# Optimization experiments

Hardware: AMD Instinct MI355X
Metric: run time of the kernel (lower is better)

The kernel has to match this reference:

```python
import jax, jax.numpy as jnp
import numpy as np

ROUTER_TEMP = 1.0
SCALING = 16.0 / 8.0  # lora_alpha / r


def setup_inputs() -> dict:
    key = jax.random.key(0)
    ks = jax.random.split(key, 6)
    B, S, D, O, E, R = 4, 2048, 4096, 4096, 8, 8
    return {
        "x": jax.random.normal(ks[0], (B, S, D), dtype=jnp.float32),
        "W_base": jax.random.normal(ks[1], (O, D), dtype=jnp.float32) * 0.02,
        "b_base": jax.random.normal(ks[2], (O,), dtype=jnp.float32) * 0.02,
        "lora_A": jax.random.normal(ks[3], (E, R, D), dtype=jnp.float32) * 0.02,
        "lora_B": jax.random.normal(ks[4], (E, O, R), dtype=jnp.float32) * 0.02,
        "router_W": jax.random.normal(ks[5], (E, D), dtype=jnp.float32) * 0.02,
        "router_b": jnp.zeros((E,), dtype=jnp.float32),
    }


def reference(x, W_base, b_base, lora_A, lora_B, router_W, router_b):
    # Base linear: [B,S,D] @ [D,O] + b -> [B,S,O]
    result = jnp.einsum("bsd,od->bso", x, W_base) + b_base

    # Router over mean-pooled sequence: [B,D] -> [B,E]
    x_router = x.mean(axis=1)
    logits = jnp.einsum("bd,ed->be", x_router, router_W) + router_b
    weights = jax.nn.softmax(logits / ROUTER_TEMP, axis=-1)  # [B,E]

    # Per-expert LoRA: down-project to small r, weight by router, up-project.
    h = jnp.einsum("bsd,erd->bser", x, lora_A)            # [B,S,E,r] (small)
    hw = h * weights[:, None, :, None]                      # router-weighted
    lora_out = jnp.einsum("bser,eor->bso", hw, lora_B)     # [B,S,O]

    return result + lora_out * SCALING
```

## Files before the change

kernel.cpp:

```cpp
#include <hip/hip_runtime.h>
#include <hip/hip_bf16.h>


typedef unsigned short u16;
typedef __attribute__((ext_vector_type(8))) short short8;
typedef __attribute__((ext_vector_type(8))) unsigned short u16x8;
typedef __attribute__((ext_vector_type(4))) float f32x4;

#define AS1(p) ((const __attribute__((address_space(1))) void*)(p))
#define AS3(p) ((__attribute__((address_space(3))) void*)(p))

constexpr int KM   = 4224;
constexpr int NOUT = 4096;

__device__ __forceinline__ u16 f2bf(float f) {
    union { float f; unsigned int u; } v; v.f = f;
    unsigned int r = v.u + 0x7fffu + ((v.u >> 16) & 1u);
    return (u16)(r >> 16);
}

__global__ __launch_bounds__(256) void k_convx(const float* __restrict__ x,
                                               u16* __restrict__ Xext,
                                               float* __restrict__ colpart) {
    const int t = threadIdx.x;
    const int row0 = (blockIdx.x >> 7) * 2048 + (blockIdx.x & 127) * 16;
    float4 cs[4] = {{0,0,0,0},{0,0,0,0},{0,0,0,0},{0,0,0,0}};
    for (int r = 0; r < 16; ++r) {
        size_t roff = (size_t)(row0 + r) * 4096;
        #pragma unroll
        for (int g = 0; g < 2; ++g) {
            int col = g * 2048 + t * 8;
            const float4* p = (const float4*)(x + roff + col);
            float4 v0 = p[0], v1 = p[1];
            cs[2*g].x += v0.x; cs[2*g].y += v0.y; cs[2*g].z += v0.z; cs[2*g].w += v0.w;
            cs[2*g+1].x += v1.x; cs[2*g+1].y += v1.y; cs[2*g+1].z += v1.z; cs[2*g+1].w += v1.w;
            u16x8 o;
            o[0]=f2bf(v0.x); o[1]=f2bf(v0.y); o[2]=f2bf(v0.z); o[3]=f2bf(v0.w);
            o[4]=f2bf(v1.x); o[5]=f2bf(v1.y); o[6]=f2bf(v1.z); o[7]=f2bf(v1.w);
            *(u16x8*)(Xext + (size_t)(row0 + r) * KM + col) = o;
        }
    }
    float* cp = colpart + (size_t)blockIdx.x * 4096;
    #pragma unroll
    for (int g = 0; g < 2; ++g) {
        *(float4*)(cp + g * 2048 + t * 8)     = cs[2*g];
        *(float4*)(cp + g * 2048 + t * 8 + 4) = cs[2*g+1];
    }
}

__global__ __launch_bounds__(256) void k_red(const float* __restrict__ colpart,
                                             float* __restrict__ colsum) {
    const int b = blockIdx.x >> 4;
    const int col = (blockIdx.x & 15) * 256 + threadIdx.x;
    const float* p = colpart + (size_t)b * 128 * 4096 + col;
    float acc = 0.f;
    #pragma unroll 4
    for (int sc = 0; sc < 128; ++sc) acc += p[(size_t)sc * 4096];
    colsum[b * 4096 + col] = acc;
}

__global__ __launch_bounds__(256) void k_lgt(const float* __restrict__ colsum,
                                             const float* __restrict__ rW,
                                             float* __restrict__ logits) {
    const int b = blockIdx.x >> 3, e = blockIdx.x & 7;
    const int t = threadIdx.x;
    const float4* cp = (const float4*)(colsum + b * 4096 + t * 16);
    const float4* wp = (const float4*)(rW + e * 4096 + t * 16);
    float acc = 0.f;
    #pragma unroll
    for (int j = 0; j < 4; ++j) {
        float4 c = cp[j], w = wp[j];
        acc += c.x * w.x + c.y * w.y + c.z * w.z + c.w * w.w;
    }
    __shared__ float red[256];
    red[t] = acc;
    __syncthreads();
    for (int off = 128; off > 0; off >>= 1) {
        if (t < off) red[t] += red[t + off];
        __syncthreads();
    }
    if (t == 0) logits[b * 8 + e] = red[0];
}

__global__ void k_conv8(const float* __restrict__ src, u16* __restrict__ dst) {
    size_t t = (size_t)blockIdx.x * 256 + threadIdx.x;
    size_t base = t * 8;
    size_t row = base >> 12;
    int col = (int)(base & 4095);
    const float4* s = (const float4*)(src + base);
    float4 v0 = s[0], v1 = s[1];
    u16x8 o;
    o[0]=f2bf(v0.x); o[1]=f2bf(v0.y); o[2]=f2bf(v0.z); o[3]=f2bf(v0.w);
    o[4]=f2bf(v1.x); o[5]=f2bf(v1.y); o[6]=f2bf(v1.z); o[7]=f2bf(v1.w);
    *(u16x8*)(dst + row * KM + col) = o;
}

__global__ void k_wlora(const float* __restrict__ lb, u16* __restrict__ Wext) {
    int f = blockIdx.x * 256 + threadIdx.x;
    int e = f >> 15, o = (f >> 3) & 4095, r = f & 7;
    Wext[(size_t)o * KM + 4096 + e * 8 + r] = f2bf(lb[f]);
    Wext[(size_t)(f >> 6) * KM + 4160 + (f & 63)] = 0;
}

__global__ void k_abf(const float* __restrict__ la, u16* __restrict__ Abf) {
    int f = blockIdx.x * 256 + threadIdx.x;
    Abf[f] = f2bf(la[f]);
}

__global__ __launch_bounds__(256) void k_hgemm(const u16* __restrict__ Xb,
                                               const u16* __restrict__ Ab,
                                               const float* __restrict__ logits,
                                               const float* __restrict__ rb,
                                               u16* __restrict__ Hout) {
    __shared__ u16 As[8 * 1024];
    __shared__ u16 Bs[8 * 2048];
    __shared__ float Red[4 * 2048];
    __shared__ float wscL[8];
    const int tid = threadIdx.x, lane = tid & 63, w = tid >> 6;
    const int m0 = blockIdx.x * 32;
    const int b = blockIdx.x >> 6;

    if (tid < 8) {
        float l[8], mx = -1e30f;
        #pragma unroll
        for (int j = 0; j < 8; ++j) {
            l[j] = logits[b * 8 + j] * (1.0f / 2048.0f) + rb[j];
            mx = fmaxf(mx, l[j]);
        }
        float s = 0.f;
        #pragma unroll
        for (int j = 0; j < 8; ++j) s += expf(l[j] - mx);
        wscL[tid] = 2.0f * expf(l[tid] - mx) / s;
    }
    asm volatile("s_waitcnt vmcnt(0)" ::: "memory");

    f32x4 acc[2][4] = {};
    const int kbase = w * 1024;

    auto issue = [&](int it, int buf) {
        const int kt = kbase + it * 32;
        u16* Aw = As + (w * 2 + buf) * 1024;
        u16* Bw = Bs + (w * 2 + buf) * 2048;
        #pragma unroll
        for (int i = 0; i < 2; ++i) {
            int f = lane + i * 64;
            __builtin_amdgcn_global_load_lds(
                AS1(Xb + (size_t)(m0 + (f >> 2)) * KM + kt + (f & 3) * 8),
                AS3(Aw + f * 8), 16, 0, 0);
        }
        #pragma unroll
        for (int i = 0; i < 4; ++i) {
            int f = lane + i * 64;
            __builtin_amdgcn_global_load_lds(
                AS1(Ab + (size_t)(f >> 2) * 4096 + kt + (f & 3) * 8),
                AS3(Bw + f * 8), 16, 0, 0);
        }
    };

    issue(0, 0);
    for (int it = 0; it < 32; ++it) {
        const int buf = it & 1;
        if (it + 1 < 32) {
            issue(it + 1, buf ^ 1);
            asm volatile("s_waitcnt vmcnt(6)" ::: "memory");
        } else {
            asm volatile("s_waitcnt vmcnt(0)" ::: "memory");
        }
        const u16* Aw = As + (w * 2 + buf) * 1024;
        const u16* Bw = Bs + (w * 2 + buf) * 2048;
        short8 af[2], bfr[4];
        #pragma unroll
        for (int mi = 0; mi < 2; ++mi)
            af[mi] = *(const short8*)(Aw + (mi * 16 + (lane & 15)) * 32 + (lane >> 4) * 8);
        #pragma unroll
        for (int nj = 0; nj < 4; ++nj)
            bfr[nj] = *(const short8*)(Bw + (nj * 16 + (lane & 15)) * 32 + (lane >> 4) * 8);
        #pragma unroll
        for (int mi = 0; mi < 2; ++mi)
            #pragma unroll
            for (int nj = 0; nj < 4; ++nj)
                acc[mi][nj] = __builtin_amdgcn_mfma_f32_16x16x32_bf16(af[mi], bfr[nj], acc[mi][nj], 0, 0, 0);
        asm volatile("" ::: "memory");
    }

    const int quad = lane >> 4, lcol = lane & 15;
    #pragma unroll
    for (int mi = 0; mi < 2; ++mi)
        #pragma unroll
        for (int nj = 0; nj < 4; ++nj)
            #pragma unroll
            for (int r = 0; r < 4; ++r)
                Red[w * 2048 + (mi * 16 + quad * 4 + r) * 64 + nj * 16 + lcol] = acc[mi][nj][r];
    __syncthreads();

    const int o = tid * 8, row = o >> 6, col = o & 63;
    float s0=0,s1=0,s2=0,s3=0,s4=0,s5=0,s6=0,s7=0;
    #pragma unroll
    for (int ww = 0; ww < 4; ++ww) {
        const float4* p = (const float4*)(Red + ww * 2048 + o);
        float4 v0 = p[0], v1 = p[1];
        s0+=v0.x; s1+=v0.y; s2+=v0.z; s3+=v0.w;
        s4+=v1.x; s5+=v1.y; s6+=v1.z; s7+=v1.w;
    }
    const float wgt = wscL[col >> 3];
    u16x8 out;
    out[0]=f2bf(s0*wgt); out[1]=f2bf(s1*wgt); out[2]=f2bf(s2*wgt); out[3]=f2bf(s3*wgt);
    out[4]=f2bf(s4*wgt); out[5]=f2bf(s5*wgt); out[6]=f2bf(s6*wgt); out[7]=f2bf(s7*wgt);
    *(u16x8*)(Hout + (size_t)(m0 + row) * KM + 4096 + col) = out;
    u16x8 zz = {0,0,0,0,0,0,0,0};
    *(u16x8*)(Hout + (size_t)(m0 + (tid >> 3)) * KM + 4160 + (tid & 7) * 8) = zz;
}


#define LDB_(bufB) do { \
    const char* bp_ = ldsc + bBaseB + (bufB); \
    _Pragma("unroll") \
    for (int nj_ = 0; nj_ < 4; ++nj_) { \
        bf[nj_][0] = *(const short8*)(bp_ + nj_ * 2048 + rdk0); \
        bf[nj_][1] = *(const short8*)(bp_ + nj_ * 2048 + rdk1); \
    } \
} while (0)

#define LDA_(bufB, pq) do { \
    const char* ap_ = ldsc + aBaseB + (bufB) + (pq) * 4096; \
    af[0][0] = *(const short8*)(ap_ + rdk0); \
    af[0][1] = *(const short8*)(ap_ + rdk1); \
    af[1][0] = *(const short8*)(ap_ + 2048 + rdk0); \
    af[1][1] = *(const short8*)(ap_ + 2048 + rdk1); \
} while (0)

#define MFMA_(pq) do { \
    __builtin_amdgcn_s_barrier(); \
    asm volatile("s_waitcnt lgkmcnt(0)" ::: "memory"); \
    __builtin_amdgcn_sched_barrier(0); \
    __builtin_amdgcn_s_setprio(1); \
    _Pragma("unroll") \
    for (int k_ = 0; k_ < 2; ++k_) \
        _Pragma("unroll") \
        for (int q_ = 0; q_ < 2; ++q_) \
            _Pragma("unroll") \
            for (int nj_ = 0; nj_ < 4; ++nj_) \
                acc[(pq)*2+q_][nj_] = __builtin_amdgcn_mfma_f32_16x16x32_bf16(af[q_][k_], bf[nj_][k_], acc[(pq)*2+q_][nj_], 0, 0, 0); \
    __builtin_amdgcn_s_setprio(0); \
    __builtin_amdgcn_sched_barrier(0); \
} while (0)

#define ENDPH_() __builtin_amdgcn_s_barrier()
#define VM_(n)   asm volatile("s_waitcnt vmcnt(" #n ")" ::: "memory")

__global__ __launch_bounds__(512, 2) void k_main(const u16* __restrict__ A, const u16* __restrict__ B,
                                                 const float* __restrict__ bias, float* __restrict__ C) {
    __shared__ __align__(16) u16 lds[65536];
    const char* ldsc = (const char*)lds;
    const int tid = threadIdx.x;
    const int lane = tid & 63;
    const int w = tid >> 6;
    const int wm = w >> 2;
    const int wn = w & 3;
    const int lr = lane & 15, hi = lane >> 4;

    const int bid = blockIdx.x;
    const int swz = (bid & 7) * 64 + (bid >> 3);
    const int m0 = (swz >> 4) * 256;
    const int n0 = (swz & 15) * 256;

    const int csw = (lr & 7) << 4;
    const int rdk0 = lr * 128 + ((hi * 16) ^ csw);
    const int rdk1 = lr * 128 + ((64 + hi * 16) ^ csw);
    const int aBaseB = wm * 16384;
    const int bBaseB = 32768 + (wn >> 1) * 16384 + (wn & 1) * 8192;

    const int srow = tid >> 3;
    const int scol = ((tid & 7) ^ ((tid >> 3) & 7)) * 8;
    const int so0 = srow * KM + scol;
    const int so1 = (64 + srow) * KM + scol;
    const u16* Am0 = A + (size_t)m0 * KM;
    const u16* Am1 = A + (size_t)(m0 + 128) * KM;
    const u16* Bm0 = B + (size_t)n0 * KM;
    const u16* Bm1 = B + (size_t)(n0 + 128) * KM;
    u16* ldst = lds + tid * 8;

    auto stageB = [&](const u16* src, int t, int regionEl) {
        __builtin_amdgcn_global_load_lds(AS1(src + so0 + t * 64), AS3(ldst + regionEl), 16, 0, 0);
        __builtin_amdgcn_global_load_lds(AS1(src + so1 + t * 64), AS3(ldst + regionEl + 4096), 16, 0, 0);
    };
    auto stageA = [&](int t, int bufEl, int which) {
        const size_t ro = (size_t)(which * 64) * KM;
        __builtin_amdgcn_global_load_lds(AS1(Am0 + ro + so0 + t * 64),
                                         AS3(ldst + bufEl + which * 4096), 16, 0, 0);
        __builtin_amdgcn_global_load_lds(AS1(Am1 + ro + so0 + t * 64),
                                         AS3(ldst + bufEl + 8192 + which * 4096), 16, 0, 0);
    };

    f32x4 acc[8][4] = {};

    stageB(Bm0, 0, 16384);
    stageB(Bm1, 0, 24576);
    stageA(0, 0, 0);
    stageA(0, 0, 1);
    stageB(Bm0, 1, 32768 + 16384);
    stageB(Bm1, 1, 32768 + 24576);
    VM_(6);
    __builtin_amdgcn_s_barrier();

    #pragma unroll 1
    for (int i = 0; i < 33; ++i) {
        const int t = i * 2;
        const bool nl = (i < 32);
        short8 af[2][2];
        short8 bf[4][2];
        LDB_(0); LDA_(0, 0);
        stageA(t + 1, 32768, 0);
        MFMA_(0); ENDPH_();
        LDA_(0, 1);
        stageA(t + 1, 32768, 1);
        MFMA_(1); VM_(8); ENDPH_();
        LDA_(0, 2);
        if (nl) stageB(Bm0, t + 2, 16384);
        MFMA_(2); ENDPH_();
        LDA_(0, 3);
        if (nl) stageB(Bm1, t + 2, 24576);
        MFMA_(3);
        if (nl) { VM_(6); } else { VM_(2); }
        ENDPH_();
        LDB_(65536); LDA_(65536, 0);
        if (nl) stageA(t + 2, 0, 0);
        MFMA_(0); ENDPH_();
        LDA_(65536, 1);
        if (nl) stageA(t + 2, 0, 1);
        MFMA_(1);
        if (nl) { VM_(8); } else { VM_(0); }
        ENDPH_();
        LDA_(65536, 2);
        if (nl) stageB(Bm0, t + 3, 32768 + 16384);
        MFMA_(2); ENDPH_();
        LDA_(65536, 3);
        if (nl) stageB(Bm1, t + 3, 32768 + 24576);
        MFMA_(3);
        if (nl) { VM_(6); }
        ENDPH_();
    }

    const int colb = n0 + wn * 64 + lr;
    const int rowb = m0 + wm * 128 + hi * 4;
    #pragma unroll
    for (int nj = 0; nj < 4; ++nj) {
        const int col = colb + nj * 16;
        const float bv = bias[col];
        #pragma unroll
        for (int mi = 0; mi < 8; ++mi) {
            float* Cp = C + (size_t)(rowb + mi * 16) * NOUT + col;
            #pragma unroll
            for (int r = 0; r < 4; ++r)
                Cp[(size_t)r * NOUT] = acc[mi][nj][r] + bv;
        }
    }
}

extern "C" void kernel_launch(void* const* d_in, const int* in_sizes, int n_in,
                              void* d_out, int out_size, void* d_ws, size_t ws_size,
                              hipStream_t stream) {
    const float* x  = (const float*)d_in[0];
    const float* Wb = (const float*)d_in[1];
    const float* bb = (const float*)d_in[2];
    const float* lA = (const float*)d_in[3];
    const float* lB = (const float*)d_in[4];
    const float* rW = (const float*)d_in[5];
    const float* rb = (const float*)d_in[6];
    float* out = (float*)d_out;

    char* ws = (char*)d_ws;
    float* logits = (float*)ws;
    u16* Abf      = (u16*)(ws + 256);
    u16* Xext     = (u16*)(ws + 524800);
    u16* Wext     = (u16*)(ws + 524800 + 69206016ULL);
    float* colpart = (float*)Wext;
    float* colsum  = (float*)((char*)Wext + (16u << 20));

    k_abf   <<<1024, 256, 0, stream>>>(lA, Abf);
    k_convx <<<512,  256, 0, stream>>>(x, Xext, colpart);
    k_red   <<<64,   256, 0, stream>>>(colpart, colsum);
    k_lgt   <<<32,   256, 0, stream>>>(colsum, rW, logits);
    k_hgemm <<<256,  256, 0, stream>>>(Xext, Abf, logits, rb, Xext);
    k_conv8 <<<8192, 256, 0, stream>>>(Wb, Wext);
    k_wlora <<<1024, 256, 0, stream>>>(lB, Wext);
    k_main  <<<512,  512, 0, stream>>>(Xext, Wext, bb, out);
}
```

Baseline: 552.0 us.

## Switch main GEMM to 32x32x16 MFMA tiles and double convx grid

The main bf16 GEMM's inner loop now issues 32x32x16 MFMA instructions instead of 16x16x32. LDS fragment reads, accumulator layout and the epilogue store mapping are reworked to match. The aim is fewer MFMA issues and fewer LDS fragment loads per tile, which raises arithmetic intensity per wave. Separately, the x-conversion kernel now uses 1024 blocks of 8 rows instead of 512 blocks of 16, for more parallelism, at the cost of a longer column-partial reduction and a larger colpart buffer.

```diff
diff --git a/kernel.cpp b/kernel.cpp
--- a/kernel.cpp
+++ b/kernel.cpp
@@ -6,6 +6,7 @@
 typedef __attribute__((ext_vector_type(8))) short short8;
 typedef __attribute__((ext_vector_type(8))) unsigned short u16x8;
 typedef __attribute__((ext_vector_type(4))) float f32x4;
+typedef __attribute__((ext_vector_type(16))) float f32x16;
 
 #define AS1(p) ((const __attribute__((address_space(1))) void*)(p))
 #define AS3(p) ((__attribute__((address_space(3))) void*)(p))
@@ -23,9 +24,9 @@
                                                u16* __restrict__ Xext,
                                                float* __restrict__ colpart) {
     const int t = threadIdx.x;
-    const int row0 = (blockIdx.x >> 7) * 2048 + (blockIdx.x & 127) * 16;
+    const int row0 = (blockIdx.x >> 8) * 2048 + (blockIdx.x & 255) * 8;
     float4 cs[4] = {{0,0,0,0},{0,0,0,0},{0,0,0,0},{0,0,0,0}};
-    for (int r = 0; r < 16; ++r) {
+    for (int r = 0; r < 8; ++r) {
         size_t roff = (size_t)(row0 + r) * 4096;
         #pragma unroll
         for (int g = 0; g < 2; ++g) {
@@ -52,10 +53,10 @@
                                              float* __restrict__ colsum) {
     const int b = blockIdx.x >> 4;
     const int col = (blockIdx.x & 15) * 256 + threadIdx.x;
-    const float* p = colpart + (size_t)b * 128 * 4096 + col;
+    const float* p = colpart + (size_t)b * 256 * 4096 + col;
     float acc = 0.f;
-    #pragma unroll 4
-    for (int sc = 0; sc < 128; ++sc) acc += p[(size_t)sc * 4096];
+    #pragma unroll 8
+    for (int sc = 0; sc < 256; ++sc) acc += p[(size_t)sc * 4096];
     colsum[b * 4096 + col] = acc;
 }
 
@@ -215,18 +216,17 @@
 #define LDB_(bufB) do { \
     const char* bp_ = ldsc + bBaseB + (bufB); \
     _Pragma("unroll") \
-    for (int nj_ = 0; nj_ < 4; ++nj_) { \
-        bf[nj_][0] = *(const short8*)(bp_ + nj_ * 2048 + rdk0); \
-        bf[nj_][1] = *(const short8*)(bp_ + nj_ * 2048 + rdk1); \
-    } \
+    for (int nj_ = 0; nj_ < 2; ++nj_) \
+        _Pragma("unroll") \
+        for (int ks_ = 0; ks_ < 4; ++ks_) \
+            bf[nj_][ks_] = *(const short8*)(bp_ + nj_ * 4096 + ardk[ks_]); \
 } while (0)
 
 #define LDA_(bufB, pq) do { \
     const char* ap_ = ldsc + aBaseB + (bufB) + (pq) * 4096; \
-    af[0][0] = *(const short8*)(ap_ + rdk0); \
-    af[0][1] = *(const short8*)(ap_ + rdk1); \
-    af[1][0] = *(const short8*)(ap_ + 2048 + rdk0); \
-    af[1][1] = *(const short8*)(ap_ + 2048 + rdk1); \
+    _Pragma("unroll") \
+    for (int ks_ = 0; ks_ < 4; ++ks_) \
+        af[ks_] = *(const short8*)(ap_ + ardk[ks_]); \
 } while (0)
 
 #define MFMA_(pq) do { \
@@ -235,12 +235,10 @@
     __builtin_amdgcn_sched_barrier(0); \
     __builtin_amdgcn_s_setprio(1); \
     _Pragma("unroll") \
-    for (int k_ = 0; k_ < 2; ++k_) \
+    for (int ks_ = 0; ks_ < 4; ++ks_) \
         _Pragma("unroll") \
-        for (int q_ = 0; q_ < 2; ++q_) \
-            _Pragma("unroll") \
-            for (int nj_ = 0; nj_ < 4; ++nj_) \
-                acc[(pq)*2+q_][nj_] = __builtin_amdgcn_mfma_f32_16x16x32_bf16(af[q_][k_], bf[nj_][k_], acc[(pq)*2+q_][nj_], 0, 0, 0); \
+        for (int nj_ = 0; nj_ < 2; ++nj_) \
+            acc[(pq)][nj_] = __builtin_amdgcn_mfma_f32_32x32x16_bf16(af[ks_], bf[nj_][ks_], acc[(pq)][nj_], 0, 0, 0); \
     __builtin_amdgcn_s_setprio(0); \
     __builtin_amdgcn_sched_barrier(0); \
 } while (0)
@@ -257,16 +255,20 @@
     const int w = tid >> 6;
     const int wm = w >> 2;
     const int wn = w & 3;
-    const int lr = lane & 15, hi = lane >> 4;
 
     const int bid = blockIdx.x;
     const int swz = (bid & 7) * 64 + (bid >> 3);
     const int m0 = (swz >> 4) * 256;
     const int n0 = (swz & 15) * 256;
 
-    const int csw = (lr & 7) << 4;
-    const int rdk0 = lr * 128 + ((hi * 16) ^ csw);
-    const int rdk1 = lr * 128 + ((64 + hi * 16) ^ csw);
+    const int l31 = lane & 31, hi32 = lane >> 5;
+    const int csw = (lane & 7) << 4;
+    const int ardk[4] = {
+        l31 * 128 + ((0 * 32 + hi32 * 16) ^ csw),
+        l31 * 128 + ((1 * 32 + hi32 * 16) ^ csw),
+        l31 * 128 + ((2 * 32 + hi32 * 16) ^ csw),
+        l31 * 128 + ((3 * 32 + hi32 * 16) ^ csw),
+    };
     const int aBaseB = wm * 16384;
     const int bBaseB = 32768 + (wn >> 1) * 16384 + (wn & 1) * 8192;
 
@@ -292,7 +294,7 @@
                                          AS3(ldst + bufEl + 8192 + which * 4096), 16, 0, 0);
     };
 
-    f32x4 acc[8][4] = {};
+    f32x16 acc[4][2] = {};
 
     stageB(Bm0, 0, 16384);
     stageB(Bm1, 0, 24576);
@@ -307,8 +309,8 @@
     for (int i = 0; i < 33; ++i) {
         const int t = i * 2;
         const bool nl = (i < 32);
-        short8 af[2][2];
-        short8 bf[4][2];
+        short8 af[4];
+        short8 bf[2][4];
         LDB_(0); LDA_(0, 0);
         stageA(t + 1, 32768, 0);
         MFMA_(0); ENDPH_();
@@ -341,18 +343,21 @@
         ENDPH_();
     }
 
-    const int colb = n0 + wn * 64 + lr;
-    const int rowb = m0 + wm * 128 + hi * 4;
-    #pragma unroll
-    for (int nj = 0; nj < 4; ++nj) {
-        const int col = colb + nj * 16;
+    const int colb = n0 + wn * 64 + l31;
+    const int rowb = m0 + wm * 128 + hi32 * 4;
+    #pragma unroll
+    for (int nj = 0; nj < 2; ++nj) {
+        const int col = colb + nj * 32;
         const float bv = bias[col];
         #pragma unroll
-        for (int mi = 0; mi < 8; ++mi) {
-            float* Cp = C + (size_t)(rowb + mi * 16) * NOUT + col;
+        for (int mi = 0; mi < 4; ++mi) {
             #pragma unroll
-            for (int r = 0; r < 4; ++r)
-                Cp[(size_t)r * NOUT] = acc[mi][nj][r] + bv;
+            for (int g = 0; g < 4; ++g) {
+                float* Cp = C + (size_t)(rowb + mi * 32 + g * 8) * NOUT + col;
+                #pragma unroll
+                for (int j = 0; j < 4; ++j)
+                    Cp[(size_t)j * NOUT] = acc[mi][nj][g * 4 + j] + bv;
+            }
         }
     }
 }
@@ -375,10 +380,10 @@
     u16* Xext     = (u16*)(ws + 524800);
     u16* Wext     = (u16*)(ws + 524800 + 69206016ULL);
     float* colpart = (float*)Wext;
-    float* colsum  = (float*)((char*)Wext + (16u << 20));
+    float* colsum  = (float*)((char*)Wext + (20u << 20));
 
     k_abf   <<<1024, 256, 0, stream>>>(lA, Abf);
-    k_convx <<<512,  256, 0, stream>>>(x, Xext, colpart);
+    k_convx <<<1024, 256, 0, stream>>>(x, Xext, colpart);
     k_red   <<<64,   256, 0, stream>>>(colpart, colsum);
     k_lgt   <<<32,   256, 0, stream>>>(colsum, rW, logits);
     k_hgemm <<<256,  256, 0, stream>>>(Xext, Abf, logits, rb, Xext);
```

Result: slower. 571.6 us (+3.6%).

## Restructure main GEMM loop into k-split half phases with reordered staging

Applied to the files above, without the earlier changes.

Reorganizes the main GEMM inner loop so that each phase loads one k-slice of B and a half of A (four 16-row fragments) and runs 16 MFMAs, instead of two k-slices over quarter tiles. Global-to-LDS staging of B for the next tile moves into the loop rather than the prologue. Explicit lgkmcnt waits and sched_barriers are dropped, leaving the compiler to schedule LDS reads. The reduction kernel unroll is also raised. The intent is to cut register pressure and rebalance the overlap between loads and MFMAs. The risk is less prefetch distance and compiler-chosen waits that may serialize.

```diff
diff --git a/kernel.cpp b/kernel.cpp
--- a/kernel.cpp
+++ b/kernel.cpp
@@ -54,7 +54,7 @@
     const int col = (blockIdx.x & 15) * 256 + threadIdx.x;
     const float* p = colpart + (size_t)b * 128 * 4096 + col;
     float acc = 0.f;
-    #pragma unroll 4
+    #pragma unroll 8
     for (int sc = 0; sc < 128; ++sc) acc += p[(size_t)sc * 4096];
     colsum[b * 4096 + col] = acc;
 }
@@ -212,37 +212,29 @@
 }
 
 
-#define LDB_(bufB) do { \
+#define LDBk_(bufB, rdk) do { \
     const char* bp_ = ldsc + bBaseB + (bufB); \
     _Pragma("unroll") \
-    for (int nj_ = 0; nj_ < 4; ++nj_) { \
-        bf[nj_][0] = *(const short8*)(bp_ + nj_ * 2048 + rdk0); \
-        bf[nj_][1] = *(const short8*)(bp_ + nj_ * 2048 + rdk1); \
-    } \
+    for (int nj_ = 0; nj_ < 4; ++nj_) \
+        bf[nj_] = *(const short8*)(bp_ + nj_ * 2048 + (rdk)); \
 } while (0)
 
-#define LDA_(bufB, pq) do { \
-    const char* ap_ = ldsc + aBaseB + (bufB) + (pq) * 4096; \
-    af[0][0] = *(const short8*)(ap_ + rdk0); \
-    af[0][1] = *(const short8*)(ap_ + rdk1); \
-    af[1][0] = *(const short8*)(ap_ + 2048 + rdk0); \
-    af[1][1] = *(const short8*)(ap_ + 2048 + rdk1); \
+#define LDAh_(bufB, h, rdk) do { \
+    const char* ap_ = ldsc + aBaseB + (bufB) + (h) * 8192; \
+    _Pragma("unroll") \
+    for (int q_ = 0; q_ < 4; ++q_) \
+        af[q_] = *(const short8*)(ap_ + q_ * 2048 + (rdk)); \
 } while (0)
 
-#define MFMA_(pq) do { \
+#define MFMAh_(h) do { \
     __builtin_amdgcn_s_barrier(); \
-    asm volatile("s_waitcnt lgkmcnt(0)" ::: "memory"); \
-    __builtin_amdgcn_sched_barrier(0); \
     __builtin_amdgcn_s_setprio(1); \
     _Pragma("unroll") \
-    for (int k_ = 0; k_ < 2; ++k_) \
+    for (int q_ = 0; q_ < 4; ++q_) \
         _Pragma("unroll") \
-        for (int q_ = 0; q_ < 2; ++q_) \
-            _Pragma("unroll") \
-            for (int nj_ = 0; nj_ < 4; ++nj_) \
-                acc[(pq)*2+q_][nj_] = __builtin_amdgcn_mfma_f32_16x16x32_bf16(af[q_][k_], bf[nj_][k_], acc[(pq)*2+q_][nj_], 0, 0, 0); \
+        for (int nj_ = 0; nj_ < 4; ++nj_) \
+            acc[(h)*4+q_][nj_] = __builtin_amdgcn_mfma_f32_16x16x32_bf16(af[q_], bf[nj_], acc[(h)*4+q_][nj_], 0, 0, 0); \
     __builtin_amdgcn_s_setprio(0); \
-    __builtin_amdgcn_sched_barrier(0); \
 } while (0)
 
 #define ENDPH_() __builtin_amdgcn_s_barrier()
@@ -298,46 +290,43 @@
     stageB(Bm1, 0, 24576);
     stageA(0, 0, 0);
     stageA(0, 0, 1);
-    stageB(Bm0, 1, 32768 + 16384);
-    stageB(Bm1, 1, 32768 + 24576);
-    VM_(6);
+    VM_(2);
     __builtin_amdgcn_s_barrier();
+
+    short8 af[4];
+    short8 bf[4];
 
     #pragma unroll 1
     for (int i = 0; i < 33; ++i) {
         const int t = i * 2;
         const bool nl = (i < 32);
-        short8 af[2][2];
-        short8 bf[4][2];
-        LDB_(0); LDA_(0, 0);
+        LDBk_(0, rdk0); LDAh_(0, 0, rdk0);
+        stageB(Bm0, t + 1, 32768 + 16384);
+        stageB(Bm1, t + 1, 32768 + 24576);
+        MFMAh_(0);
+        VM_(4); ENDPH_();
+        LDAh_(0, 1, rdk0);
         stageA(t + 1, 32768, 0);
-        MFMA_(0); ENDPH_();
-        LDA_(0, 1);
         stageA(t + 1, 32768, 1);
-        MFMA_(1); VM_(8); ENDPH_();
-        LDA_(0, 2);
-        if (nl) stageB(Bm0, t + 2, 16384);
-        MFMA_(2); ENDPH_();
-        LDA_(0, 3);
-        if (nl) stageB(Bm1, t + 2, 24576);
-        MFMA_(3);
-        if (nl) { VM_(6); } else { VM_(2); }
+        MFMAh_(1); ENDPH_();
+        LDBk_(0, rdk1); LDAh_(0, 0, rdk1);
+        MFMAh_(0); ENDPH_();
+        LDAh_(0, 1, rdk1);
+        MFMAh_(1);
+        VM_(2); ENDPH_();
+        LDBk_(65536, rdk0); LDAh_(65536, 0, rdk0);
+        if (nl) { stageB(Bm0, t + 2, 16384); stageB(Bm1, t + 2, 24576); }
+        MFMAh_(0);
+        if (nl) { VM_(4); } else { VM_(0); }
         ENDPH_();
-        LDB_(65536); LDA_(65536, 0);
-        if (nl) stageA(t + 2, 0, 0);
-        MFMA_(0); ENDPH_();
-        LDA_(65536, 1);
-        if (nl) stageA(t + 2, 0, 1);
-        MFMA_(1);
-        if (nl) { VM_(8); } else { VM_(0); }
-        ENDPH_();
-        LDA_(65536, 2);
-        if (nl) stageB(Bm0, t + 3, 32768 + 16384);
-        MFMA_(2); ENDPH_();
-        LDA_(65536, 3);
-        if (nl) stageB(Bm1, t + 3, 32768 + 24576);
-        MFMA_(3);
-        if (nl) { VM_(6); }
+        LDAh_(65536, 1, rdk0);
+        if (nl) { stageA(t + 2, 0, 0); stageA(t + 2, 0, 1); }
+        MFMAh_(1); ENDPH_();
+        LDBk_(65536, rdk1); LDAh_(65536, 0, rdk1);
+        MFMAh_(0); ENDPH_();
+        LDAh_(65536, 1, rdk1);
+        MFMAh_(1);
+        if (nl) { VM_(2); }
         ENDPH_();
     }
 
```

Result: no change. 542.9 us (-1.6%).
